# Kernel optimization log

Hardware: AMD Instinct MI355X
Metric: run time of the kernel (lower is better)

The kernel has to match this reference:

```python
import jax, jax.numpy as jnp
import numpy as np

ROUTING_ITERS = 3

def setup_inputs() -> dict:
    key = jax.random.key(0)
    k1, k2 = jax.random.split(key)
    B, N, C, OUT, IN = 256, 1152, 10, 16, 8
    x = jax.random.normal(k1, (B, N, IN), dtype=jnp.float32)
    W = jax.random.normal(k2, (1, N, C, OUT, IN), dtype=jnp.float32)
    return {"x": x, "W": W}

def _squash_elementwise(s):
    # Faithful to original: torch.norm over trailing singleton dim == |s|,
    # so squash reduces to |s|^2/(1+|s|^2) * s/|s| = s*|s|/(1+s^2) elementwise.
    return s * jnp.abs(s) / (1.0 + s * s)

def reference(x, W):
    B = x.shape[0]
    N, C = W.shape[1], W.shape[2]
    # u_hat[b,n,k,o] = sum_i W[0,n,k,o,i] * x[b,n,i]
    u_hat = jnp.einsum('nkoi,bni->bnko', W[0], x)
    b_ij = jnp.zeros((N, C), dtype=x.dtype)  # shared across batch, as in original
    v = None
    for it in range(ROUTING_ITERS):
        c_ij = jax.nn.softmax(b_ij, axis=1)            # softmax over capsules (dim=2 orig)
        s_j = jnp.einsum('nk,bnko->bko', c_ij, u_hat)  # sum over route nodes
        v = _squash_elementwise(s_j)                    # [B, C, OUT]
        if it < ROUTING_ITERS - 1:
            # a_ij[b,n,k] = u_hat[b,n,k,:] . v[b,k,:]; mean over batch
            a = jnp.einsum('bnko,bko->nk', u_hat, v) / B
            b_ij = b_ij + a
    return v[..., None]  # [B, C, OUT, 1] matching v_j.squeeze(1)
```

## Files before the change

kernel.cpp:

```cpp
#include <hip/hip_runtime.h>
#include <math.h>

#define B 256
#define N 1152
#define C_ 10
#define OUT 16
#define IN 8
#define KO 160
#define MB 32
#define NC 36
#define NCH 32
#define KG 2
#define NKG 5
#define NPAIR (NCH*NKG)
#define PAIR_PER_XCD (NPAIR/8)
#define XS_STRIDE (NC*IN + 8)

__global__ __launch_bounds__(256, 4) void k_s_partial(
    const float* __restrict__ x, const float* __restrict__ W,
    const float* __restrict__ c, float* __restrict__ partial)
{
    __shared__ float xs[MB][XS_STRIDE];
    __shared__ float cs[NC][KG];

    const int tid = threadIdx.x;
    const int id  = blockIdx.x;
    const int g   = id & 7;
    const int q   = id >> 3;
    const int bt  = q & 7;
    const int pp_ = q >> 3;
    const int pair = g * PAIR_PER_XCD + pp_;
    const int ch  = pair & 31;
    const int kg  = pair >> 5;
    const int b0  = bt * MB;
    const int n0  = ch * NC;
    const int k0  = kg * KG;

    for (int idx = tid; idx < MB * (NC * IN / 4); idx += 256) {
        int bl = idx / (NC * IN / 4);
        int r  = idx - bl * (NC * IN / 4);
        float4 val = *(const float4*)(x + (size_t)(b0 + bl) * (N * IN) + (size_t)n0 * IN + r * 4);
        *(float4*)(&xs[bl][r * 4]) = val;
    }
    if (c) {
        for (int idx = tid; idx < NC * KG; idx += 256) {
            int nl = idx >> 1, kk = idx & 1;
            cs[nl][kk] = c[(size_t)(n0 + nl) * C_ + (k0 + kk)];
        }
    }
    __syncthreads();

    const int o    = tid & 15;
    const int bgrp = tid >> 4;

    float acc00 = 0.f, acc01 = 0.f, acc10 = 0.f, acc11 = 0.f;

    const float* Wbase = W + (size_t)n0 * (KO * IN) + (size_t)(k0 * OUT + o) * IN;

#pragma unroll 2
    for (int nl = 0; nl < NC; ++nl) {
        float4 xa0 = *(const float4*)(&xs[bgrp][nl * IN]);
        float4 xa1 = *(const float4*)(&xs[bgrp][nl * IN + 4]);
        float4 xb0 = *(const float4*)(&xs[bgrp + 16][nl * IN]);
        float4 xb1 = *(const float4*)(&xs[bgrp + 16][nl * IN + 4]);
        const float* Wn = Wbase + (size_t)nl * (KO * IN);
        float cw0 = c ? cs[nl][0] : 0.1f;
        float cw1 = c ? cs[nl][1] : 0.1f;

        {
            const float4* wp = (const float4*)(Wn);
            float4 w0 = wp[0], w1 = wp[1];
            float da = w0.x*xa0.x + w0.y*xa0.y + w0.z*xa0.z + w0.w*xa0.w
                     + w1.x*xa1.x + w1.y*xa1.y + w1.z*xa1.z + w1.w*xa1.w;
            float db = w0.x*xb0.x + w0.y*xb0.y + w0.z*xb0.z + w0.w*xb0.w
                     + w1.x*xb1.x + w1.y*xb1.y + w1.z*xb1.z + w1.w*xb1.w;
            acc00 += cw0 * da;  acc10 += cw0 * db;
        }
        {
            const float4* wp = (const float4*)(Wn + OUT * IN);
            float4 w0 = wp[0], w1 = wp[1];
            float da = w0.x*xa0.x + w0.y*xa0.y + w0.z*xa0.z + w0.w*xa0.w
                     + w1.x*xa1.x + w1.y*xa1.y + w1.z*xa1.z + w1.w*xa1.w;
            float db = w0.x*xb0.x + w0.y*xb0.y + w0.z*xb0.z + w0.w*xb0.w
                     + w1.x*xb1.x + w1.y*xb1.y + w1.z*xb1.z + w1.w*xb1.w;
            acc01 += cw1 * da;  acc11 += cw1 * db;
        }
    }

    float* ppa = partial + (size_t)ch * (B * KO) + (size_t)(b0 + bgrp) * KO + (size_t)k0 * OUT + o;
    float* ppb = ppa + (size_t)16 * KO;
    ppa[0]   = acc00;  ppa[OUT] = acc01;
    ppb[0]   = acc10;  ppb[OUT] = acc11;
}

__global__ __launch_bounds__(256) void k_reduce_squash(
    const float* __restrict__ partial, float* __restrict__ v, float* __restrict__ out)
{
    __shared__ float red[256];
    const int tid = threadIdx.x;
    const int e   = blockIdx.x * 64 + (tid >> 2);
    const int q   = tid & 3;
    float s = 0.f;
#pragma unroll
    for (int ch = 0; ch < NCH / 4; ++ch)
        s += partial[(size_t)(q * (NCH / 4) + ch) * (B * KO) + e];
    red[tid] = s;
    __syncthreads();
    if (q == 0) {
        s = red[tid] + red[tid + 1] + red[tid + 2] + red[tid + 3];
        float vv = s * fabsf(s) / (1.f + s * s);
        v[e] = vv;
        if (out) out[e] = vv;
    }
}

__global__ __launch_bounds__(256) void k_a(
    const float* __restrict__ x, const float* __restrict__ W,
    const float* __restrict__ v, float* __restrict__ bij, int accumulate)
{
    const int n = blockIdx.x;
    const int tid = threadIdx.x;

    __shared__ float Wl[KO][IN + 1];
    __shared__ float xsl[B][IN];
    __shared__ float red[256][C_];

    for (int idx = tid; idx < KO * IN; idx += 256)
        Wl[idx >> 3][idx & 7] = W[(size_t)n * (KO * IN) + idx];
    for (int idx = tid; idx < B * IN / 4; idx += 256) {
        int bb = idx >> 1, r = idx & 1;
        *(float4*)(&xsl[bb][r * 4]) = *(const float4*)(x + (size_t)bb * (N * IN) + (size_t)n * IN + r * 4);
    }
    __syncthreads();

    const int o = tid & 15;
    const int blane = tid >> 4;

    float part[C_];
#pragma unroll
    for (int k = 0; k < C_; ++k) part[k] = 0.f;

    for (int t = 0; t < B / 16; ++t) {
        int bb = blane + t * 16;
        float xv[IN];
#pragma unroll
        for (int i = 0; i < IN; ++i) xv[i] = xsl[bb][i];
        const float* vb = v + (size_t)bb * KO + o;
#pragma unroll
        for (int k = 0; k < C_; ++k) {
            const float* wp = &Wl[k * OUT + o][0];
            float d = 0.f;
#pragma unroll
            for (int i = 0; i < IN; ++i) d += wp[i] * xv[i];
            part[k] += d * vb[k * OUT];
        }
    }

#pragma unroll
    for (int k = 0; k < C_; ++k) red[tid][k] = part[k];
    __syncthreads();
    for (int off = 128; off > 0; off >>= 1) {
        if (tid < off) {
#pragma unroll
            for (int k = 0; k < C_; ++k) red[tid][k] += red[tid + off][k];
        }
        __syncthreads();
    }
    if (tid < C_) {
        float a = red[0][tid] * (1.0f / B);
        float* bp = bij + (size_t)n * C_ + tid;
        *bp = accumulate ? (*bp + a) : a;
    }
}

__global__ __launch_bounds__(256) void k_softmax(
    const float* __restrict__ bij, float* __restrict__ c)
{
    int n = blockIdx.x * 256 + threadIdx.x;
    if (n >= N) return;
    float b[C_], m = -1e30f;
#pragma unroll
    for (int k = 0; k < C_; ++k) { b[k] = bij[(size_t)n * C_ + k]; m = fmaxf(m, b[k]); }
    float s = 0.f;
#pragma unroll
    for (int k = 0; k < C_; ++k) { float e = __expf(b[k] - m); b[k] = e; s += e; }
    float inv = 1.f / s;
#pragma unroll
    for (int k = 0; k < C_; ++k) c[(size_t)n * C_ + k] = b[k] * inv;
}

extern "C" void kernel_launch(void* const* d_in, const int* in_sizes, int n_in,
                              void* d_out, int out_size, void* d_ws, size_t ws_size,
                              hipStream_t stream)
{
    const float* x = (const float*)d_in[0];
    const float* W = (const float*)d_in[1];
    float* out = (float*)d_out;
    float* ws  = (float*)d_ws;

    float* part = ws;
    float* bij  = ws + 1310720;
    float* c    = bij + 11520;
    float* v    = c + 11520;

    const int GS = 8 * PAIR_PER_XCD * 8;

    k_s_partial<<<GS, 256, 0, stream>>>(x, W, nullptr, part);
    k_reduce_squash<<<640, 256, 0, stream>>>(part, v, nullptr);
    k_a<<<N, 256, 0, stream>>>(x, W, v, bij, 0);

    k_softmax<<<5, 256, 0, stream>>>(bij, c);
    k_s_partial<<<GS, 256, 0, stream>>>(x, W, c, part);
    k_reduce_squash<<<640, 256, 0, stream>>>(part, v, nullptr);
    k_a<<<N, 256, 0, stream>>>(x, W, v, bij, 1);

    k_softmax<<<5, 256, 0, stream>>>(bij, c);
    k_s_partial<<<GS, 256, 0, stream>>>(x, W, c, part);
    k_reduce_squash<<<640, 256, 0, stream>>>(part, v, out);
}
```

Baseline: 155.9 us.

## Halve route-node chunks, double chunk count, and prefetch W one node ahead

Splits the route-node dimension into 64 chunks of 18 instead of 32 of 36, doubling the grid of the partial-sum kernel, and changes the block-to-(chunk, capsule-group) mapping so each XCD gets whole chunks across all capsule groups. The inner loop now software-prefetches the next node's W vectors into registers while computing the current one. The goal is more parallelism and hidden global-load latency. The cost is twice as many partial buffers, a larger workspace, and more reduction traffic in k_reduce_squash, whose loop still uses NCH/4 and so reads all 64 chunks.

```diff
diff --git a/kernel.cpp b/kernel.cpp
--- a/kernel.cpp
+++ b/kernel.cpp
@@ -8,8 +8,8 @@
 #define IN 8
 #define KO 160
 #define MB 32
-#define NC 36
-#define NCH 32
+#define NC 18
+#define NCH 64
 #define KG 2
 #define NKG 5
 #define NPAIR (NCH*NKG)
@@ -29,9 +29,8 @@
     const int q   = id >> 3;
     const int bt  = q & 7;
     const int pp_ = q >> 3;
-    const int pair = g * PAIR_PER_XCD + pp_;
-    const int ch  = pair & 31;
-    const int kg  = pair >> 5;
+    const int kg  = pp_ % 5;
+    const int ch  = g * (PAIR_PER_XCD / 5) + pp_ / 5;
     const int b0  = bt * MB;
     const int n0  = ch * NC;
     const int k0  = kg * KG;
@@ -57,34 +56,40 @@
 
     const float* Wbase = W + (size_t)n0 * (KO * IN) + (size_t)(k0 * OUT + o) * IN;
 
+    float4 w00 = *(const float4*)(Wbase);
+    float4 w01 = *(const float4*)(Wbase + 4);
+    float4 w10 = *(const float4*)(Wbase + OUT * IN);
+    float4 w11 = *(const float4*)(Wbase + OUT * IN + 4);
+
 #pragma unroll 2
     for (int nl = 0; nl < NC; ++nl) {
+        const int nn = (nl + 1 < NC) ? (nl + 1) : nl;
+        const float* Wn = Wbase + (size_t)nn * (KO * IN);
+        float4 p00 = *(const float4*)(Wn);
+        float4 p01 = *(const float4*)(Wn + 4);
+        float4 p10 = *(const float4*)(Wn + OUT * IN);
+        float4 p11 = *(const float4*)(Wn + OUT * IN + 4);
+
         float4 xa0 = *(const float4*)(&xs[bgrp][nl * IN]);
         float4 xa1 = *(const float4*)(&xs[bgrp][nl * IN + 4]);
         float4 xb0 = *(const float4*)(&xs[bgrp + 16][nl * IN]);
         float4 xb1 = *(const float4*)(&xs[bgrp + 16][nl * IN + 4]);
-        const float* Wn = Wbase + (size_t)nl * (KO * IN);
         float cw0 = c ? cs[nl][0] : 0.1f;
         float cw1 = c ? cs[nl][1] : 0.1f;
 
-        {
-            const float4* wp = (const float4*)(Wn);
-            float4 w0 = wp[0], w1 = wp[1];
-            float da = w0.x*xa0.x + w0.y*xa0.y + w0.z*xa0.z + w0.w*xa0.w
-                     + w1.x*xa1.x + w1.y*xa1.y + w1.z*xa1.z + w1.w*xa1.w;
-            float db = w0.x*xb0.x + w0.y*xb0.y + w0.z*xb0.z + w0.w*xb0.w
-                     + w1.x*xb1.x + w1.y*xb1.y + w1.z*xb1.z + w1.w*xb1.w;
-            acc00 += cw0 * da;  acc10 += cw0 * db;
-        }
-        {
-            const float4* wp = (const float4*)(Wn + OUT * IN);
-            float4 w0 = wp[0], w1 = wp[1];
-            float da = w0.x*xa0.x + w0.y*xa0.y + w0.z*xa0.z + w0.w*xa0.w
-                     + w1.x*xa1.x + w1.y*xa1.y + w1.z*xa1.z + w1.w*xa1.w;
-            float db = w0.x*xb0.x + w0.y*xb0.y + w0.z*xb0.z + w0.w*xb0.w
-                     + w1.x*xb1.x + w1.y*xb1.y + w1.z*xb1.z + w1.w*xb1.w;
-            acc01 += cw1 * da;  acc11 += cw1 * db;
-        }
+        float da0 = w00.x*xa0.x + w00.y*xa0.y + w00.z*xa0.z + w00.w*xa0.w
+                  + w01.x*xa1.x + w01.y*xa1.y + w01.z*xa1.z + w01.w*xa1.w;
+        float db0 = w00.x*xb0.x + w00.y*xb0.y + w00.z*xb0.z + w00.w*xb0.w
+                  + w01.x*xb1.x + w01.y*xb1.y + w01.z*xb1.z + w01.w*xb1.w;
+        float da1 = w10.x*xa0.x + w10.y*xa0.y + w10.z*xa0.z + w10.w*xa0.w
+                  + w11.x*xa1.x + w11.y*xa1.y + w11.z*xa1.z + w11.w*xa1.w;
+        float db1 = w10.x*xb0.x + w10.y*xb0.y + w10.z*xb0.z + w10.w*xb0.w
+                  + w11.x*xb1.x + w11.y*xb1.y + w11.z*xb1.z + w11.w*xb1.w;
+
+        acc00 += cw0 * da0;  acc10 += cw0 * db0;
+        acc01 += cw1 * da1;  acc11 += cw1 * db1;
+
+        w00 = p00; w01 = p01; w10 = p10; w11 = p11;
     }
 
     float* ppa = partial + (size_t)ch * (B * KO) + (size_t)(b0 + bgrp) * KO + (size_t)k0 * OUT + o;
@@ -199,7 +204,7 @@
     float* ws  = (float*)d_ws;
 
     float* part = ws;
-    float* bij  = ws + 1310720;
+    float* bij  = ws + 2621440;
     float* c    = bij + 11520;
     float* v    = c + 11520;
 
```

New measurement: 147.5 us. 1.06x faster.
